# Performance work log

Measured on AMD Instinct MI355X. Metric: run time of the kernel, lower is better.

## Reference

```python
import jax, jax.numpy as jnp
import numpy as np

H = 1024      # hidden_size
NH = 16       # num_heads
DH = H // NH  # size_per_head
RV = 32       # relative_vocab_size
B, S = 1, 2048


def setup_inputs() -> dict:
    key = jax.random.key(0)
    ks = jax.random.split(key, 12)
    std = 0.02
    inp = {
        'x': jax.random.normal(ks[0], (B, S, H), jnp.float32),
        'att_mask': jnp.ones((B, S, S), jnp.int32),
        'relative_att_ids': jax.random.randint(ks[1], (B, S, S), 0, RV),
        'Wq': jax.random.normal(ks[2], (H, H), jnp.float32) * std,
        'bq': jnp.zeros((H,), jnp.float32),
        'Wk': jax.random.normal(ks[3], (H, H), jnp.float32) * std,
        'bk': jnp.zeros((H,), jnp.float32),
        'Wv': jax.random.normal(ks[4], (H, H), jnp.float32) * std,
        'bv': jnp.zeros((H,), jnp.float32),
        'rel_emb': jax.random.normal(ks[5], (RV, NH, DH), jnp.float32) * 0.5,
        'rel_bias': jnp.zeros((RV, NH), jnp.float32),
        'Wo': jax.random.normal(ks[6], (H, H), jnp.float32) * std,
        'bo': jnp.zeros((H,), jnp.float32),
    }
    return inp


def reference(x, att_mask, relative_att_ids, Wq, bq, Wk, bk, Wv, bv,
              rel_emb, rel_bias, Wo, bo):
    b, s, _ = x.shape
    # multi-head projections: [b, s, nh, dh]
    q = (x @ Wq + bq).reshape(b, s, NH, DH)
    k = (x @ Wk + bk).reshape(b, s, NH, DH)
    v = (x @ Wv + bv).reshape(b, s, NH, DH)

    # content scores: [b, q, k, h]
    content = jnp.einsum('bqhd,bkhd->bqkh', q, k)

    # relative scores over vocab: [b, q, r, h], then gather per key position
    all_rel = jnp.einsum('bqhd,rhd->bqrh', q, rel_emb) + rel_bias
    rel_scores = jnp.take_along_axis(all_rel, relative_att_ids[..., None], axis=2)

    scores = (content + rel_scores) / jnp.sqrt(jnp.asarray(DH, x.dtype))
    scores = scores + (-10000.0) * (1.0 - att_mask[..., None].astype(scores.dtype))

    probs = jax.nn.softmax(scores, axis=2)  # softmax over key dim (axis=-2)
    ctx = jnp.einsum('bqkh,bkhd->bqhd', probs, v).reshape(b, s, H)
    return ctx @ Wo + bo
```

## Files before the change

kernel.cpp:

```cpp
#include <hip/hip_runtime.h>
#include <hip/hip_bf16.h>

#define S 2048
#define H 1024
#define NH 16
#define DH 64
#define RV 32
#define BK 32

typedef __hip_bfloat16 bf16;
typedef short bf16x8 __attribute__((ext_vector_type(8)));
typedef float f32x4 __attribute__((ext_vector_type(4)));

__device__ __forceinline__ float b2f(bf16 v) { return __bfloat162float(v); }
__device__ __forceinline__ unsigned short f2bbits(float x) {
    __hip_bfloat16 b = __float2bfloat16(x);
    return *reinterpret_cast<unsigned short*>(&b);
}
__device__ __forceinline__ float ldf(const void* p, int i, int f) {
    return f ? ((const float*)p)[i] : b2f(((const bf16*)p)[i]);
}
__device__ __forceinline__ void gl_lds16(const bf16* g, bf16* l) {
    __builtin_amdgcn_global_load_lds(
        (const __attribute__((address_space(1))) void*)g,
        (__attribute__((address_space(3))) void*)l,
        16, 0, 0);
}

__global__ void detect_dtype(const unsigned int* __restrict__ xw,
                             int* __restrict__ flag)
{
    __shared__ int cnt;
    if (threadIdx.x == 0) cnt = 0;
    __syncthreads();
    unsigned int w = xw[threadIdx.x];
    unsigned int ex = ((w & 0xffffu) >> 7) & 0xffu;
    int big = (ex > 134u) ? 1 : 0;
    #pragma unroll
    for (int off = 32; off > 0; off >>= 1) big += __shfl_xor(big, off, 64);
    if ((threadIdx.x & 63) == 0) atomicAdd(&cnt, big);
    __syncthreads();
    if (threadIdx.x == 0) *flag = (cnt > 60) ? 1 : 0;
}

__global__ __launch_bounds__(256) void convert_x(
    const void* __restrict__ x, bf16* __restrict__ xb,
    const int* __restrict__ flag)
{
    const int i = (blockIdx.x * 256 + threadIdx.x) * 4;
    if (*flag) {
        float4 v = ((const float4*)x)[i >> 2];
        ushort4 o;
        o.x = f2bbits(v.x); o.y = f2bbits(v.y);
        o.z = f2bbits(v.z); o.w = f2bbits(v.w);
        *(ushort4*)&xb[i] = o;
    } else {
        ((ushort4*)xb)[i >> 2] = ((const ushort4*)x)[i >> 2];
    }
}

__global__ __launch_bounds__(256) void wtrans(
    const void* __restrict__ W0, const void* __restrict__ W1,
    const void* __restrict__ W2, const void* __restrict__ W3,
    bf16* __restrict__ T0, bf16* __restrict__ T1,
    bf16* __restrict__ T2, bf16* __restrict__ T3,
    const int* __restrict__ flag)
{
    const void* W; bf16* T;
    switch (blockIdx.z) {
        case 0:  W = W0; T = T0; break;
        case 1:  W = W1; T = T1; break;
        case 2:  W = W2; T = T2; break;
        default: W = W3; T = T3; break;
    }
    const int f = *flag;
    __shared__ unsigned short Ts[64][68];
    const int t = threadIdx.x;
    const int tx = t & 15, ty = t >> 4;
    const int n0 = blockIdx.x * 64;
    const int k0 = blockIdx.y * 64;
    #pragma unroll
    for (int it = 0; it < 4; ++it) {
        int k = ty + it * 16;
        int base = (k0 + k) * H + n0 + tx * 4;
        #pragma unroll
        for (int e = 0; e < 4; ++e)
            Ts[k][tx * 4 + e] = f2bbits(ldf(W, base + e, f));
    }
    __syncthreads();
    #pragma unroll
    for (int it = 0; it < 4; ++it) {
        int n = ty + it * 16;
        ushort4 o;
        o.x = Ts[tx * 4 + 0][n];
        o.y = Ts[tx * 4 + 1][n];
        o.z = Ts[tx * 4 + 2][n];
        o.w = Ts[tx * 4 + 3][n];
        *(ushort4*)&T[(size_t)(n0 + n) * H + k0 + tx * 4] = o;
    }
}

__global__ __launch_bounds__(256) void vtrans(
    const bf16* __restrict__ Vb, bf16* __restrict__ VT)
{
    __shared__ unsigned short Ts[64][68];
    const int t = threadIdx.x;
    const int tx = t & 15, ty = t >> 4;
    const int s0 = blockIdx.x * 64;
    const int h0 = blockIdx.y * 64;
    #pragma unroll
    for (int it = 0; it < 4; ++it) {
        int s = ty + it * 16;
        *(ushort4*)&Ts[s][tx * 4] =
            *(const ushort4*)&Vb[(size_t)(s0 + s) * H + h0 + tx * 4];
    }
    __syncthreads();
    #pragma unroll
    for (int it = 0; it < 4; ++it) {
        int hh = ty + it * 16;
        ushort4 o;
        o.x = Ts[tx * 4 + 0][hh];
        o.y = Ts[tx * 4 + 1][hh];
        o.z = Ts[tx * 4 + 2][hh];
        o.w = Ts[tx * 4 + 3][hh];
        *(ushort4*)&VT[(size_t)(h0 + hh) * S + s0 + tx * 4] = o;
    }
}

__device__ __forceinline__ void gemm128_bt(
    const bf16* __restrict__ A, const bf16* __restrict__ BT,
    f32x4 (&acc)[4][4])
{
    const int tid = threadIdx.x;
    const int w = tid >> 6, lane = tid & 63;
    const int l15 = lane & 15, quad = lane >> 4;
    const int wm = (w & 1) * 64, wn = (w >> 1) * 64;
    const int rowb = blockIdx.y * 128;
    const int colb = blockIdx.x * 128;

    __shared__ bf16 As[128 * BK];
    __shared__ bf16 Bs[128 * BK];

    for (int kb = 0; kb < H; kb += BK) {
        #pragma unroll
        for (int j = 0; j < 2; ++j) {
            int i = j * 256 + w * 64 + lane;
            gl_lds16(&A[(size_t)(rowb + (i >> 2)) * H + kb + (i & 3) * 8],
                     &As[(size_t)(j * 256 + w * 64) * 8]);
            gl_lds16(&BT[(size_t)(colb + (i >> 2)) * H + kb + (i & 3) * 8],
                     &Bs[(size_t)(j * 256 + w * 64) * 8]);
        }
        __syncthreads();

        bf16x8 af[4], bfr[4];
        #pragma unroll
        for (int mt = 0; mt < 4; ++mt)
            af[mt] = *(const bf16x8*)&As[(wm + mt * 16 + l15) * BK + quad * 8];
        #pragma unroll
        for (int nt = 0; nt < 4; ++nt)
            bfr[nt] = *(const bf16x8*)&Bs[(wn + nt * 16 + l15) * BK + quad * 8];
        #pragma unroll
        for (int mt = 0; mt < 4; ++mt)
            #pragma unroll
            for (int nt = 0; nt < 4; ++nt)
                acc[mt][nt] = __builtin_amdgcn_mfma_f32_16x16x32_bf16(
                    af[mt], bfr[nt], acc[mt][nt], 0, 0, 0);
        __syncthreads();
    }
}

__global__ __launch_bounds__(256) void qkv_mfma(
    const bf16* __restrict__ xb,
    const bf16* __restrict__ WTq, const bf16* __restrict__ WTk,
    const bf16* __restrict__ WTv,
    const void* __restrict__ bq, const void* __restrict__ bk,
    const void* __restrict__ bv,
    bf16* __restrict__ Qb, bf16* __restrict__ Kb, bf16* __restrict__ Vb,
    const int* __restrict__ flag)
{
    const bf16* BT; const void* bias; bf16* out;
    if (blockIdx.z == 0)      { BT = WTq; bias = bq; out = Qb; }
    else if (blockIdx.z == 1) { BT = WTk; bias = bk; out = Kb; }
    else                      { BT = WTv; bias = bv; out = Vb; }
    const int f = *flag;

    f32x4 acc[4][4];
    #pragma unroll
    for (int a = 0; a < 4; ++a)
        #pragma unroll
        for (int b = 0; b < 4; ++b) acc[a][b] = (f32x4)0.f;

    gemm128_bt(xb, BT, acc);

    const int tid = threadIdx.x;
    const int w = tid >> 6, lane = tid & 63;
    const int l15 = lane & 15, quad = lane >> 4;
    const int wm = (w & 1) * 64, wn = (w >> 1) * 64;
    const int rowb = blockIdx.y * 128;
    const int colb = blockIdx.x * 128;

    float bvv[4];
    #pragma unroll
    for (int nt = 0; nt < 4; ++nt)
        bvv[nt] = ldf(bias, colb + wn + nt * 16 + l15, f);

    #pragma unroll
    for (int mt = 0; mt < 4; ++mt)
        #pragma unroll
        for (int nt = 0; nt < 4; ++nt)
            #pragma unroll
            for (int r = 0; r < 4; ++r) {
                int m = rowb + wm + mt * 16 + quad * 4 + r;
                int n = colb + wn + nt * 16 + l15;
                out[(size_t)m * H + n] = __float2bfloat16(acc[mt][nt][r] + bvv[nt]);
            }
}

__global__ __launch_bounds__(256) void out_mfma(
    const bf16* __restrict__ Cb, const bf16* __restrict__ WoT,
    const void* __restrict__ bias, void* __restrict__ out,
    const int* __restrict__ flag)
{
    const int f = *flag;
    f32x4 acc[4][4];
    #pragma unroll
    for (int a = 0; a < 4; ++a)
        #pragma unroll
        for (int b = 0; b < 4; ++b) acc[a][b] = (f32x4)0.f;

    gemm128_bt(Cb, WoT, acc);

    const int tid = threadIdx.x;
    const int w = tid >> 6, lane = tid & 63;
    const int l15 = lane & 15, quad = lane >> 4;
    const int wm = (w & 1) * 64, wn = (w >> 1) * 64;
    const int rowb = blockIdx.y * 128;
    const int colb = blockIdx.x * 128;

    float bvv[4];
    #pragma unroll
    for (int nt = 0; nt < 4; ++nt)
        bvv[nt] = ldf(bias, colb + wn + nt * 16 + l15, f);

    #pragma unroll
    for (int mt = 0; mt < 4; ++mt)
        #pragma unroll
        for (int nt = 0; nt < 4; ++nt)
            #pragma unroll
            for (int r = 0; r < 4; ++r) {
                int m = rowb + wm + mt * 16 + quad * 4 + r;
                int n = colb + wn + nt * 16 + l15;
                float v = acc[mt][nt][r] + bvv[nt];
                if (f) ((float*)out)[(size_t)m * H + n] = v;
                else   ((bf16*)out)[(size_t)m * H + n] = __float2bfloat16(v);
            }
}

__global__ __launch_bounds__(256) void attn_mfma(
    const bf16* __restrict__ Qb, const bf16* __restrict__ Kb,
    const bf16* __restrict__ VT,
    const void* __restrict__ rel_emb, const void* __restrict__ rel_bias,
    const int* __restrict__ att_mask, const int* __restrict__ rel_ids,
    bf16* __restrict__ Cb, const int* __restrict__ flag)
{
    const int h = blockIdx.y;
    const int q0 = blockIdx.x * 64;
    const int tid = threadIdx.x;
    const int w = tid >> 6;
    const int lane = tid & 63;
    const int l15 = lane & 15;
    const int quad = lane >> 4;
    const int f = *flag;

    __shared__ short Qs[64][72];
    __shared__ short Ks[64][72];
    __shared__ short Vs[64][72];
    __shared__ short Ps[64][72];
    __shared__ float Bias[64][64];
    __shared__ float Rl[64][33];
    __shared__ short Es[32][72];
    __shared__ float Rbias[32];

    for (int slot = tid; slot < 512; slot += 256) {
        int q = slot >> 3, c = slot & 7;
        *(uint4*)&Qs[q][c * 8] = *(const uint4*)&Qb[(q0 + q) * H + h * DH + c * 8];
    }
    {
        int r = tid >> 3, c8 = (tid & 7) * 8;
        if (f) {
            const float* src = (const float*)rel_emb + (r * NH + h) * DH + c8;
            ushort4 o0, o1;
            o0.x = f2bbits(src[0]); o0.y = f2bbits(src[1]);
            o0.z = f2bbits(src[2]); o0.w = f2bbits(src[3]);
            o1.x = f2bbits(src[4]); o1.y = f2bbits(src[5]);
            o1.z = f2bbits(src[6]); o1.w = f2bbits(src[7]);
            *(ushort4*)&Es[r][c8] = o0;
            *(ushort4*)&Es[r][c8 + 4] = o1;
        } else {
            *(uint4*)&Es[r][c8] =
                *(const uint4*)((const bf16*)rel_emb + (r * NH + h) * DH + c8);
        }
        if (tid < RV) Rbias[tid] = ldf(rel_bias, tid * NH + h, f);
    }
    __syncthreads();

    bf16x8 aq0 = *(const bf16x8*)&Qs[w * 16 + l15][quad * 8];
    bf16x8 aq1 = *(const bf16x8*)&Qs[w * 16 + l15][32 + quad * 8];

    #pragma unroll
    for (int nt = 0; nt < 2; ++nt) {
        bf16x8 be0 = *(const bf16x8*)&Es[nt * 16 + l15][quad * 8];
        bf16x8 be1 = *(const bf16x8*)&Es[nt * 16 + l15][32 + quad * 8];
        f32x4 c = (f32x4)0.f;
        c = __builtin_amdgcn_mfma_f32_16x16x32_bf16(aq0, be0, c, 0, 0, 0);
        c = __builtin_amdgcn_mfma_f32_16x16x32_bf16(aq1, be1, c, 0, 0, 0);
        float rb = Rbias[nt * 16 + l15];
        #pragma unroll
        for (int r = 0; r < 4; ++r)
            Rl[w * 16 + quad * 4 + r][nt * 16 + l15] = c[r] + rb;
    }
    __syncthreads();

    f32x4 O[4];
    float mrow[4], lrow[4];
    #pragma unroll
    for (int i = 0; i < 4; ++i) { O[i] = (f32x4)0.f; mrow[i] = -1e30f; lrow[i] = 0.f; }

    for (int kt = 0; kt < S; kt += 64) {
        for (int slot = tid; slot < 512; slot += 256) {
            int r = slot >> 3, c = slot & 7;
            *(uint4*)&Ks[r][c * 8] = *(const uint4*)&Kb[(kt + r) * H + h * DH + c * 8];
            *(uint4*)&Vs[r][c * 8] = *(const uint4*)&VT[(size_t)(h * DH + r) * S + kt + c * 8];
        }
        {
            int q = tid >> 2, kg = (tid & 3) * 16;
            const int4* ridp = (const int4*)(rel_ids + (q0 + q) * S + kt + kg);
            const int4* mskp = (const int4*)(att_mask + (q0 + q) * S + kt + kg);
            #pragma unroll
            for (int v4 = 0; v4 < 4; ++v4) {
                int4 rid = ridp[v4];
                int4 msk = mskp[v4];
                Bias[q][kg + v4 * 4 + 0] = Rl[q][rid.x] * 0.125f - 10000.0f * (1.0f - (float)msk.x);
                Bias[q][kg + v4 * 4 + 1] = Rl[q][rid.y] * 0.125f - 10000.0f * (1.0f - (float)msk.y);
                Bias[q][kg + v4 * 4 + 2] = Rl[q][rid.z] * 0.125f - 10000.0f * (1.0f - (float)msk.z);
                Bias[q][kg + v4 * 4 + 3] = Rl[q][rid.w] * 0.125f - 10000.0f * (1.0f - (float)msk.w);
            }
        }
        __syncthreads();

        f32x4 sc[4];
        #pragma unroll
        for (int nt = 0; nt < 4; ++nt) {
            bf16x8 bk0 = *(const bf16x8*)&Ks[nt * 16 + l15][quad * 8];
            bf16x8 bk1 = *(const bf16x8*)&Ks[nt * 16 + l15][32 + quad * 8];
            f32x4 c = (f32x4)0.f;
            c = __builtin_amdgcn_mfma_f32_16x16x32_bf16(aq0, bk0, c, 0, 0, 0);
            c = __builtin_amdgcn_mfma_f32_16x16x32_bf16(aq1, bk1, c, 0, 0, 0);
            sc[nt] = c;
        }
        #pragma unroll
        for (int nt = 0; nt < 4; ++nt)
            #pragma unroll
            for (int r = 0; r < 4; ++r)
                sc[nt][r] = sc[nt][r] * 0.125f + Bias[w * 16 + quad * 4 + r][nt * 16 + l15];

        float alpha[4];
        #pragma unroll
        for (int r = 0; r < 4; ++r) {
            float v = fmaxf(fmaxf(sc[0][r], sc[1][r]), fmaxf(sc[2][r], sc[3][r]));
            v = fmaxf(v, __shfl_xor(v, 1, 64));
            v = fmaxf(v, __shfl_xor(v, 2, 64));
            v = fmaxf(v, __shfl_xor(v, 4, 64));
            v = fmaxf(v, __shfl_xor(v, 8, 64));
            float mnew = fmaxf(mrow[r], v);
            alpha[r] = __expf(mrow[r] - mnew);
            mrow[r] = mnew;
        }
        float rsum[4] = {0.f, 0.f, 0.f, 0.f};
        #pragma unroll
        for (int nt = 0; nt < 4; ++nt)
            #pragma unroll
            for (int r = 0; r < 4; ++r) {
                float p = __expf(sc[nt][r] - mrow[r]);
                sc[nt][r] = p;
                rsum[r] += p;
            }
        #pragma unroll
        for (int r = 0; r < 4; ++r) {
            float v = rsum[r];
            v += __shfl_xor(v, 1, 64);
            v += __shfl_xor(v, 2, 64);
            v += __shfl_xor(v, 4, 64);
            v += __shfl_xor(v, 8, 64);
            lrow[r] = lrow[r] * alpha[r] + v;
            #pragma unroll
            for (int dt = 0; dt < 4; ++dt) O[dt][r] *= alpha[r];
        }

        #pragma unroll
        for (int nt = 0; nt < 4; ++nt)
            #pragma unroll
            for (int r = 0; r < 4; ++r)
                ((unsigned short*)&Ps[w * 16 + quad * 4 + r][nt * 16 + l15])[0] = f2bbits(sc[nt][r]);

        bf16x8 ap0 = *(const bf16x8*)&Ps[w * 16 + l15][quad * 8];
        bf16x8 ap1 = *(const bf16x8*)&Ps[w * 16 + l15][32 + quad * 8];
        #pragma unroll
        for (int dt = 0; dt < 4; ++dt) {
            bf16x8 bv0 = *(const bf16x8*)&Vs[dt * 16 + l15][quad * 8];
            bf16x8 bv1 = *(const bf16x8*)&Vs[dt * 16 + l15][32 + quad * 8];
            O[dt] = __builtin_amdgcn_mfma_f32_16x16x32_bf16(ap0, bv0, O[dt], 0, 0, 0);
            O[dt] = __builtin_amdgcn_mfma_f32_16x16x32_bf16(ap1, bv1, O[dt], 0, 0, 0);
        }
        __syncthreads();
    }

    #pragma unroll
    for (int r = 0; r < 4; ++r) {
        int q = q0 + w * 16 + quad * 4 + r;
        float inv = 1.0f / lrow[r];
        #pragma unroll
        for (int dt = 0; dt < 4; ++dt)
            Cb[(size_t)q * H + h * DH + dt * 16 + l15] = __float2bfloat16(O[dt][r] * inv);
    }
}

extern "C" void kernel_launch(void* const* d_in, const int* in_sizes, int n_in,
                              void* d_out, int out_size, void* d_ws, size_t ws_size,
                              hipStream_t stream)
{
    const void* x        = d_in[0];
    const int*  att_mask = (const int*)d_in[1];
    const int*  rel_ids  = (const int*)d_in[2];
    const void* Wq = d_in[3];
    const void* bq = d_in[4];
    const void* Wk = d_in[5];
    const void* bk = d_in[6];
    const void* Wv = d_in[7];
    const void* bv = d_in[8];
    const void* rel_emb  = d_in[9];
    const void* rel_bias = d_in[10];
    const void* Wo = d_in[11];
    const void* bo = d_in[12];

    char* p = (char*)d_ws;
    bf16* xb  = (bf16*)p; p += (size_t)S * H * 2;
    bf16* WTq = (bf16*)p; p += (size_t)H * H * 2;
    bf16* WTk = (bf16*)p; p += (size_t)H * H * 2;
    bf16* WTv = (bf16*)p; p += (size_t)H * H * 2;
    bf16* WoT = (bf16*)p; p += (size_t)H * H * 2;
    bf16* Qb  = (bf16*)p; p += (size_t)S * H * 2;
    bf16* Kb  = (bf16*)p; p += (size_t)S * H * 2;
    bf16* Vb  = (bf16*)p; p += (size_t)S * H * 2;
    bf16* VT  = (bf16*)p; p += (size_t)S * H * 2;
    bf16* Cb  = (bf16*)p; p += (size_t)S * H * 2;
    int* flag = (int*)p;

    detect_dtype<<<1, 256, 0, stream>>>((const unsigned int*)x, flag);

    convert_x<<<(S * H) / 1024, 256, 0, stream>>>(x, xb, flag);
    wtrans<<<dim3(H / 64, H / 64, 4), 256, 0, stream>>>(
        Wq, Wk, Wv, Wo, WTq, WTk, WTv, WoT, flag);

    qkv_mfma<<<dim3(H / 128, S / 128, 3), 256, 0, stream>>>(
        xb, WTq, WTk, WTv, bq, bk, bv, Qb, Kb, Vb, flag);

    vtrans<<<dim3(S / 64, H / 64), 256, 0, stream>>>(Vb, VT);

    attn_mfma<<<dim3(S / 64, NH), 256, 0, stream>>>(
        Qb, Kb, VT, rel_emb, rel_bias, att_mask, rel_ids, Cb, flag);

    out_mfma<<<dim3(H / 128, S / 128), 256, 0, stream>>>(Cb, WoT, bo, d_out, flag);
}
```

Baseline: 272.1 us.

## Pack rel ids and mask into bytes, prefetch K/V tiles, fold scale into Q

A new pre-pass packs relative ids and the attention mask into one byte per (q,k) pair, so the attention kernel reads 1 byte instead of 8 per score. The attention kernel now loads the next K/V/packed tile into registers while computing the current one, and scales Q and rel_bias by 1/8 up front instead of scaling scores. The bias staging buffer is dropped and the bias is looked up inline. LDS buffers share storage through a union, launch bounds are raised, and the grid is reordered so heads sharing a query block run adjacently and reuse the packed tile from cache. Pre-scaling Q in bf16 adds a small rounding difference, and the pack pass costs one extra full read of the S×S int inputs.

```diff
diff --git a/kernel.cpp b/kernel.cpp
--- a/kernel.cpp
+++ b/kernel.cpp
@@ -41,6 +41,21 @@
     if ((threadIdx.x & 63) == 0) atomicAdd(&cnt, big);
     __syncthreads();
     if (threadIdx.x == 0) *flag = (cnt > 60) ? 1 : 0;
+}
+
+__global__ __launch_bounds__(256) void pack_rm(
+    const int* __restrict__ rel_ids, const int* __restrict__ att_mask,
+    unsigned char* __restrict__ PBg)
+{
+    int i = blockIdx.x * 256 + threadIdx.x;
+    int4 rid = ((const int4*)rel_ids)[i];
+    int4 msk = ((const int4*)att_mask)[i];
+    uchar4 o;
+    o.x = (unsigned char)(rid.x | ((msk.x == 0) << 7));
+    o.y = (unsigned char)(rid.y | ((msk.y == 0) << 7));
+    o.z = (unsigned char)(rid.z | ((msk.z == 0) << 7));
+    o.w = (unsigned char)(rid.w | ((msk.w == 0) << 7));
+    ((uchar4*)PBg)[i] = o;
 }
 
 __global__ __launch_bounds__(256) void convert_x(
@@ -256,15 +271,15 @@
             }
 }
 
-__global__ __launch_bounds__(256) void attn_mfma(
+__global__ __launch_bounds__(256, 4) void attn_mfma(
     const bf16* __restrict__ Qb, const bf16* __restrict__ Kb,
     const bf16* __restrict__ VT,
     const void* __restrict__ rel_emb, const void* __restrict__ rel_bias,
-    const int* __restrict__ att_mask, const int* __restrict__ rel_ids,
+    const unsigned char* __restrict__ PBg,
     bf16* __restrict__ Cb, const int* __restrict__ flag)
 {
-    const int h = blockIdx.y;
-    const int q0 = blockIdx.x * 64;
+    const int h = blockIdx.x;
+    const int q0 = blockIdx.y * 64;
     const int tid = threadIdx.x;
     const int w = tid >> 6;
     const int lane = tid & 63;
@@ -272,18 +287,41 @@
     const int quad = lane >> 4;
     const int f = *flag;
 
-    __shared__ short Qs[64][72];
     __shared__ short Ks[64][72];
     __shared__ short Vs[64][72];
-    __shared__ short Ps[64][72];
-    __shared__ float Bias[64][64];
     __shared__ float Rl[64][33];
-    __shared__ short Es[32][72];
     __shared__ float Rbias[32];
+    union SharedU {
+        struct { short Qs[64][72]; short Es[32][72]; } init;
+        struct { short Ps[64][72]; unsigned char PB[64][64]; } main;
+    };
+    __shared__ SharedU U;
+
+    uint4 kp[2], vp[2], pbp;
+    {
+        #pragma unroll
+        for (int j = 0; j < 2; ++j) {
+            int slot = j * 256 + tid;
+            int r = slot >> 3, c = slot & 7;
+            kp[j] = *(const uint4*)&Kb[(size_t)r * H + h * DH + c * 8];
+            vp[j] = *(const uint4*)&VT[(size_t)(h * DH + r) * S + c * 8];
+        }
+        int pq = tid >> 2, pc = (tid & 3) * 16;
+        pbp = *(const uint4*)&PBg[(size_t)(q0 + pq) * S + pc];
+    }
 
     for (int slot = tid; slot < 512; slot += 256) {
         int q = slot >> 3, c = slot & 7;
-        *(uint4*)&Qs[q][c * 8] = *(const uint4*)&Qb[(q0 + q) * H + h * DH + c * 8];
+        uint4 raw = *(const uint4*)&Qb[(size_t)(q0 + q) * H + h * DH + c * 8];
+        const unsigned short* rs = (const unsigned short*)&raw;
+        unsigned short os[8];
+        #pragma unroll
+        for (int e = 0; e < 8; ++e) {
+            float v; *((unsigned int*)&v) = ((unsigned int)rs[e]) << 16;
+            os[e] = f2bbits(v * 0.125f);
+        }
+        *(ushort4*)&U.init.Qs[q][c * 8]     = *(ushort4*)&os[0];
+        *(ushort4*)&U.init.Qs[q][c * 8 + 4] = *(ushort4*)&os[4];
     }
     {
         int r = tid >> 3, c8 = (tid & 7) * 8;
@@ -294,23 +332,23 @@
             o0.z = f2bbits(src[2]); o0.w = f2bbits(src[3]);
             o1.x = f2bbits(src[4]); o1.y = f2bbits(src[5]);
             o1.z = f2bbits(src[6]); o1.w = f2bbits(src[7]);
-            *(ushort4*)&Es[r][c8] = o0;
-            *(ushort4*)&Es[r][c8 + 4] = o1;
+            *(ushort4*)&U.init.Es[r][c8] = o0;
+            *(ushort4*)&U.init.Es[r][c8 + 4] = o1;
         } else {
-            *(uint4*)&Es[r][c8] =
+            *(uint4*)&U.init.Es[r][c8] =
                 *(const uint4*)((const bf16*)rel_emb + (r * NH + h) * DH + c8);
         }
-        if (tid < RV) Rbias[tid] = ldf(rel_bias, tid * NH + h, f);
+        if (tid < RV) Rbias[tid] = ldf(rel_bias, tid * NH + h, f) * 0.125f;
     }
     __syncthreads();
 
-    bf16x8 aq0 = *(const bf16x8*)&Qs[w * 16 + l15][quad * 8];
-    bf16x8 aq1 = *(const bf16x8*)&Qs[w * 16 + l15][32 + quad * 8];
+    bf16x8 aq0 = *(const bf16x8*)&U.init.Qs[w * 16 + l15][quad * 8];
+    bf16x8 aq1 = *(const bf16x8*)&U.init.Qs[w * 16 + l15][32 + quad * 8];
 
     #pragma unroll
     for (int nt = 0; nt < 2; ++nt) {
-        bf16x8 be0 = *(const bf16x8*)&Es[nt * 16 + l15][quad * 8];
-        bf16x8 be1 = *(const bf16x8*)&Es[nt * 16 + l15][32 + quad * 8];
+        bf16x8 be0 = *(const bf16x8*)&U.init.Es[nt * 16 + l15][quad * 8];
+        bf16x8 be1 = *(const bf16x8*)&U.init.Es[nt * 16 + l15][32 + quad * 8];
         f32x4 c = (f32x4)0.f;
         c = __builtin_amdgcn_mfma_f32_16x16x32_bf16(aq0, be0, c, 0, 0, 0);
         c = __builtin_amdgcn_mfma_f32_16x16x32_bf16(aq1, be1, c, 0, 0, 0);
@@ -326,27 +364,29 @@
     #pragma unroll
     for (int i = 0; i < 4; ++i) { O[i] = (f32x4)0.f; mrow[i] = -1e30f; lrow[i] = 0.f; }
 
+    const int pq = tid >> 2, pc = (tid & 3) * 16;
+
     for (int kt = 0; kt < S; kt += 64) {
-        for (int slot = tid; slot < 512; slot += 256) {
+        #pragma unroll
+        for (int j = 0; j < 2; ++j) {
+            int slot = j * 256 + tid;
             int r = slot >> 3, c = slot & 7;
-            *(uint4*)&Ks[r][c * 8] = *(const uint4*)&Kb[(kt + r) * H + h * DH + c * 8];
-            *(uint4*)&Vs[r][c * 8] = *(const uint4*)&VT[(size_t)(h * DH + r) * S + kt + c * 8];
-        }
-        {
-            int q = tid >> 2, kg = (tid & 3) * 16;
-            const int4* ridp = (const int4*)(rel_ids + (q0 + q) * S + kt + kg);
-            const int4* mskp = (const int4*)(att_mask + (q0 + q) * S + kt + kg);
-            #pragma unroll
-            for (int v4 = 0; v4 < 4; ++v4) {
-                int4 rid = ridp[v4];
-                int4 msk = mskp[v4];
-                Bias[q][kg + v4 * 4 + 0] = Rl[q][rid.x] * 0.125f - 10000.0f * (1.0f - (float)msk.x);
-                Bias[q][kg + v4 * 4 + 1] = Rl[q][rid.y] * 0.125f - 10000.0f * (1.0f - (float)msk.y);
-                Bias[q][kg + v4 * 4 + 2] = Rl[q][rid.z] * 0.125f - 10000.0f * (1.0f - (float)msk.z);
-                Bias[q][kg + v4 * 4 + 3] = Rl[q][rid.w] * 0.125f - 10000.0f * (1.0f - (float)msk.w);
+            *(uint4*)&Ks[r][c * 8] = kp[j];
+            *(uint4*)&Vs[r][c * 8] = vp[j];
+        }
+        *(uint4*)&U.main.PB[pq][pc] = pbp;
+        __syncthreads();
+
+        if (kt + 64 < S) {
+            #pragma unroll
+            for (int j = 0; j < 2; ++j) {
+                int slot = j * 256 + tid;
+                int r = slot >> 3, c = slot & 7;
+                kp[j] = *(const uint4*)&Kb[(size_t)(kt + 64 + r) * H + h * DH + c * 8];
+                vp[j] = *(const uint4*)&VT[(size_t)(h * DH + r) * S + kt + 64 + c * 8];
             }
-        }
-        __syncthreads();
+            pbp = *(const uint4*)&PBg[(size_t)(q0 + pq) * S + kt + 64 + pc];
+        }
 
         f32x4 sc[4];
         #pragma unroll
@@ -361,8 +401,13 @@
         #pragma unroll
         for (int nt = 0; nt < 4; ++nt)
             #pragma unroll
-            for (int r = 0; r < 4; ++r)
-                sc[nt][r] = sc[nt][r] * 0.125f + Bias[w * 16 + quad * 4 + r][nt * 16 + l15];
+            for (int r = 0; r < 4; ++r) {
+                int row = w * 16 + quad * 4 + r;
+                unsigned char b = U.main.PB[row][nt * 16 + l15];
+                float rl = Rl[row][b & 63];
+                float mt = (b & 0x80) ? -10000.0f : 0.0f;
+                sc[nt][r] = sc[nt][r] + rl + mt;
+            }
 
         float alpha[4];
         #pragma unroll
@@ -401,10 +446,11 @@
         for (int nt = 0; nt < 4; ++nt)
             #pragma unroll
             for (int r = 0; r < 4; ++r)
-                ((unsigned short*)&Ps[w * 16 + quad * 4 + r][nt * 16 + l15])[0] = f2bbits(sc[nt][r]);
-
-        bf16x8 ap0 = *(const bf16x8*)&Ps[w * 16 + l15][quad * 8];
-        bf16x8 ap1 = *(const bf16x8*)&Ps[w * 16 + l15][32 + quad * 8];
+                ((unsigned short*)&U.main.Ps[w * 16 + quad * 4 + r][nt * 16 + l15])[0] =
+                    f2bbits(sc[nt][r]);
+
+        bf16x8 ap0 = *(const bf16x8*)&U.main.Ps[w * 16 + l15][quad * 8];
+        bf16x8 ap1 = *(const bf16x8*)&U.main.Ps[w * 16 + l15][32 + quad * 8];
         #pragma unroll
         for (int dt = 0; dt < 4; ++dt) {
             bf16x8 bv0 = *(const bf16x8*)&Vs[dt * 16 + l15][quad * 8];
@@ -454,10 +500,12 @@
     bf16* Vb  = (bf16*)p; p += (size_t)S * H * 2;
     bf16* VT  = (bf16*)p; p += (size_t)S * H * 2;
     bf16* Cb  = (bf16*)p; p += (size_t)S * H * 2;
+    unsigned char* PBg = (unsigned char*)p; p += (size_t)S * S;
     int* flag = (int*)p;
 
     detect_dtype<<<1, 256, 0, stream>>>((const unsigned int*)x, flag);
 
+    pack_rm<<<(S * S) / 1024, 256, 0, stream>>>(rel_ids, att_mask, PBg);
     convert_x<<<(S * H) / 1024, 256, 0, stream>>>(x, xb, flag);
     wtrans<<<dim3(H / 64, H / 64, 4), 256, 0, stream>>>(
         Wq, Wk, Wv, Wo, WTq, WTk, WTv, WoT, flag);
@@ -467,8 +515,8 @@
 
     vtrans<<<dim3(S / 64, H / 64), 256, 0, stream>>>(Vb, VT);
 
-    attn_mfma<<<dim3(S / 64, NH), 256, 0, stream>>>(
-        Qb, Kb, VT, rel_emb, rel_bias, att_mask, rel_ids, Cb, flag);
+    attn_mfma<<<dim3(NH, S / 64), 256, 0, stream>>>(
+        Qb, Kb, VT, rel_emb, rel_bias, PBg, Cb, flag);
 
     out_mfma<<<dim3(H / 128, S / 128), 256, 0, stream>>>(Cb, WoT, bo, d_out, flag);
 }
```

Result: no change. 276.1 us (+1.5%).
